# Kernel optimization log

Hardware: AMD Instinct MI355X
Metric: run time of the kernel (lower is better)

## Reference

```python
import jax, jax.numpy as jnp
import numpy as np

N_NODES = 50000
N_EDGES = 800000
D_IN = 128
D_HID = 128
D_OUT = 1
N_GRAPHS = 64
NEG_SLOPE = 0.2


def gat_layer(x, src, dst, W, a_src, a_dst, b, n_nodes):
    # x: [N, d_in] -> h: [N, d_hid]
    h = x @ W
    alpha_s = h @ a_src  # [N]
    alpha_d = h @ a_dst  # [N]
    e = jax.nn.leaky_relu(alpha_s[src] + alpha_d[dst], NEG_SLOPE)  # [E]
    # segment softmax over destination neighborhoods
    m = jax.ops.segment_max(e, dst, num_segments=n_nodes)
    ex = jnp.exp(e - m[dst])
    denom = jax.ops.segment_sum(ex, dst, num_segments=n_nodes)
    alpha = ex / (denom[dst] + 1e-16)  # [E]
    out = jax.ops.segment_sum(h[src] * alpha[:, None], dst, num_segments=n_nodes)
    return out + b


def setup_inputs() -> dict:
    key = jax.random.key(0)
    ks = jax.random.split(key, 16)
    x = jax.random.normal(ks[0], (N_NODES, D_IN), dtype=jnp.float32)
    edge_index = jax.random.randint(ks[1], (2, N_EDGES), 0, N_NODES, dtype=jnp.int32)
    batch = jnp.sort(jax.random.randint(ks[2], (N_NODES,), 0, N_GRAPHS, dtype=jnp.int32))
    inp = {"x": x, "edge_index": edge_index, "batch": batch}
    dims = [(D_IN, D_HID), (D_HID, D_HID), (D_HID, D_HID), (D_HID, D_HID)]
    for i, (di, dh) in enumerate(dims, 1):
        kk = jax.random.split(ks[2 + i], 4)
        s = 1.0 / np.sqrt(di)
        inp[f"W{i}"] = jax.random.uniform(kk[0], (di, dh), jnp.float32, -s, s)
        inp[f"a_src{i}"] = jax.random.uniform(kk[1], (dh,), jnp.float32, -s, s)
        inp[f"a_dst{i}"] = jax.random.uniform(kk[2], (dh,), jnp.float32, -s, s)
        inp[f"b{i}"] = jnp.zeros((dh,), jnp.float32)
    s = 1.0 / np.sqrt(D_HID)
    inp["fcW"] = jax.random.uniform(ks[10], (D_HID, D_OUT), jnp.float32, -s, s)
    inp["fcb"] = jnp.zeros((D_OUT,), jnp.float32)
    return inp


def reference(x, edge_index, batch,
              W1, a_src1, a_dst1, b1,
              W2, a_src2, a_dst2, b2,
              W3, a_src3, a_dst3, b3,
              W4, a_src4, a_dst4, b4,
              fcW, fcb):
    n = x.shape[0]
    loops = jnp.arange(n, dtype=edge_index.dtype)
    src = jnp.concatenate([edge_index[0], loops])  # add self-loops (PyG default)
    dst = jnp.concatenate([edge_index[1], loops])
    h = jax.nn.relu(gat_layer(x, src, dst, W1, a_src1, a_dst1, b1, n))
    h = jax.nn.relu(gat_layer(h, src, dst, W2, a_src2, a_dst2, b2, n))
    h = jax.nn.relu(gat_layer(h, src, dst, W3, a_src3, a_dst3, b3, n))
    h = jax.nn.relu(gat_layer(h, src, dst, W4, a_src4, a_dst4, b4, n))
    # global mean pool over graphs
    sums = jax.ops.segment_sum(h, batch, num_segments=N_GRAPHS)
    counts = jax.ops.segment_sum(jnp.ones((n,), h.dtype), batch, num_segments=N_GRAPHS)
    pooled = sums / jnp.maximum(counts, 1.0)[:, None]
    return pooled @ fcW + fcb
```

## Files before the change

kernel.cpp:

```cpp
#include <hip/hip_runtime.h>

#define N_NODES 50000
#define N_EDGES 800000
#define E_TOT (N_EDGES + N_NODES)
#define D 128
#define N_GRAPHS 64
#define NEG_SLOPE 0.2f
#define MAXDEG 256
#define SCAN_BLK 1024
#define SCAN_GRID ((N_NODES + SCAN_BLK - 1) / SCAN_BLK)

typedef _Float16 f16x8 __attribute__((ext_vector_type(8)));
typedef _Float16 f16x2 __attribute__((ext_vector_type(2)));
typedef float f32x4 __attribute__((ext_vector_type(4)));

__device__ __forceinline__ float wave_max(float v) {
  #pragma unroll
  for (int off = 32; off > 0; off >>= 1) v = fmaxf(v, __shfl_xor(v, off));
  return v;
}
__device__ __forceinline__ float wave_sum(float v) {
  #pragma unroll
  for (int off = 32; off > 0; off >>= 1) v += __shfl_xor(v, off);
  return v;
}

__global__ void k_count(const int* __restrict__ ei, int* __restrict__ cnt) {
  int e = blockIdx.x * blockDim.x + threadIdx.x;
  if (e >= E_TOT) return;
  int dst = (e < N_EDGES) ? ei[N_EDGES + e] : (e - N_EDGES);
  atomicAdd(&cnt[dst], 1);
}

__global__ __launch_bounds__(SCAN_BLK) void k_scan1(const int* __restrict__ cnt,
                                                    int* __restrict__ rowptr,
                                                    int* __restrict__ partial) {
  __shared__ int sm[SCAN_BLK];
  int i = blockIdx.x * SCAN_BLK + threadIdx.x;
  int v = (i < N_NODES) ? cnt[i] : 0;
  sm[threadIdx.x] = v;
  __syncthreads();
  #pragma unroll
  for (int off = 1; off < SCAN_BLK; off <<= 1) {
    int t = (threadIdx.x >= off) ? sm[threadIdx.x - off] : 0;
    __syncthreads();
    sm[threadIdx.x] += t;
    __syncthreads();
  }
  if (i < N_NODES) rowptr[i + 1] = sm[threadIdx.x];
  if (threadIdx.x == SCAN_BLK - 1) partial[blockIdx.x] = sm[threadIdx.x];
}

__global__ void k_scan2(int* __restrict__ partial) {
  int lane = threadIdx.x;
  int v = (lane < SCAN_GRID) ? partial[lane] : 0;
  #pragma unroll
  for (int off = 1; off < 64; off <<= 1) {
    int t = __shfl_up(v, off);
    if (lane >= off) v += t;
  }
  if (lane < SCAN_GRID) partial[lane] = v;
}

__global__ __launch_bounds__(SCAN_BLK) void k_scan3(int* __restrict__ rowptr,
                                                    const int* __restrict__ partial) {
  int i = blockIdx.x * SCAN_BLK + threadIdx.x;
  if (i == 0) rowptr[0] = 0;
  if (i < N_NODES && blockIdx.x > 0) rowptr[i + 1] += partial[blockIdx.x - 1];
}

struct WPtrs {
  const float* w[4];
  _Float16* h[4];
  _Float16* l[4];
};
__global__ __launch_bounds__(256) void k_wconv_all(WPtrs p) {
  int layer = blockIdx.x >> 6;
  int e = (blockIdx.x & 63) * 256 + threadIdx.x;
  int k = e >> 7, n = e & 127;
  float v = p.w[layer][e];
  _Float16 h = (_Float16)v;
  _Float16 lo = (_Float16)(v - (float)h);
  int idx = (n >> 4) * 2048 + (k >> 3) * 128 + (n & 15) * 8 + (k & 7);
  p.h[layer][idx] = h;
  p.l[layer][idx] = lo;
}

template <int DO_FILL>
__global__ __launch_bounds__(256) void k_gemm_mfma(const float* __restrict__ X,
                                                   const _Float16* __restrict__ Whf,
                                                   const _Float16* __restrict__ Wlf,
                                                   _Float16* __restrict__ Hh,
                                                   const float* __restrict__ asrc,
                                                   const float* __restrict__ adst,
                                                   float* __restrict__ alpha_s,
                                                   float* __restrict__ alpha_d,
                                                   const int* __restrict__ ei,
                                                   const int* __restrict__ rowptr,
                                                   int* __restrict__ fill,
                                                   int* __restrict__ col) {
  __shared__ __align__(16) _Float16 AhL[8192];
  __shared__ __align__(16) _Float16 AlL[8192];
  const int tid = threadIdx.x;
  const int l = tid & 63;
  const int w = tid >> 6;
  const int rowbase = blockIdx.x * 64;

  #pragma unroll
  for (int p = 0; p < 4; ++p) {
    int row = p * 16 + (tid >> 4);
    int k0 = (tid & 15) * 8;
    int grow = rowbase + row;
    float xv[8];
    if (grow < N_NODES) {
      float4 f0 = *reinterpret_cast<const float4*>(&X[(size_t)grow * D + k0]);
      float4 f1 = *reinterpret_cast<const float4*>(&X[(size_t)grow * D + k0 + 4]);
      xv[0] = f0.x; xv[1] = f0.y; xv[2] = f0.z; xv[3] = f0.w;
      xv[4] = f1.x; xv[5] = f1.y; xv[6] = f1.z; xv[7] = f1.w;
    } else {
      #pragma unroll
      for (int j = 0; j < 8; ++j) xv[j] = 0.f;
    }
    f16x8 ah, al;
    #pragma unroll
    for (int j = 0; j < 8; ++j) {
      ah[j] = (_Float16)xv[j];
      al[j] = (_Float16)(xv[j] - (float)ah[j]);
    }
    int idx = (((row >> 4) * 16 + (k0 >> 3)) * 16 + (row & 15)) * 8;
    *reinterpret_cast<f16x8*>(&AhL[idx]) = ah;
    *reinterpret_cast<f16x8*>(&AlL[idx]) = al;
  }
  __syncthreads();

  f32x4 acc[8];
  #pragma unroll
  for (int cc = 0; cc < 8; ++cc) acc[cc] = (f32x4){0.f, 0.f, 0.f, 0.f};

  #pragma unroll
  for (int kt = 0; kt < 4; ++kt) {
    int aidx = w * 2048 + kt * 512 + l * 8;
    f16x8 ah = *reinterpret_cast<const f16x8*>(&AhL[aidx]);
    f16x8 al = *reinterpret_cast<const f16x8*>(&AlL[aidx]);
    #pragma unroll
    for (int cc = 0; cc < 8; ++cc) {
      int bidx = cc * 2048 + kt * 512 + l * 8;
      f16x8 bh = *reinterpret_cast<const f16x8*>(&Whf[bidx]);
      f16x8 bl = *reinterpret_cast<const f16x8*>(&Wlf[bidx]);
      acc[cc] = __builtin_amdgcn_mfma_f32_16x16x32_f16(ah, bh, acc[cc], 0, 0, 0);
      acc[cc] = __builtin_amdgcn_mfma_f32_16x16x32_f16(ah, bl, acc[cc], 0, 0, 0);
      acc[cc] = __builtin_amdgcn_mfma_f32_16x16x32_f16(al, bh, acc[cc], 0, 0, 0);
    }
  }

  const int myn = l & 15;
  const int rg4 = l >> 4;
  float asv[8], adv[8];
  #pragma unroll
  for (int cc = 0; cc < 8; ++cc) {
    asv[cc] = asrc[cc * 16 + myn];
    adv[cc] = adst[cc * 16 + myn];
  }
  #pragma unroll
  for (int reg = 0; reg < 4; ++reg) {
    int grow = rowbase + w * 16 + rg4 * 4 + reg;
    float ps = 0.f, pd = 0.f;
    #pragma unroll
    for (int cc = 0; cc < 8; ++cc) {
      float v = acc[cc][reg];
      ps = fmaf(v, asv[cc], ps);
      pd = fmaf(v, adv[cc], pd);
      if (grow < N_NODES) Hh[(size_t)grow * D + cc * 16 + myn] = (_Float16)v;
    }
    #pragma unroll
    for (int off = 1; off < 16; off <<= 1) {
      ps += __shfl_xor(ps, off);
      pd += __shfl_xor(pd, off);
    }
    if (grow < N_NODES && myn == 0) {
      alpha_s[grow] = ps;
      alpha_d[grow] = pd;
    }
  }

  if (DO_FILL) {
    int stride = gridDim.x * blockDim.x;
    for (int e = blockIdx.x * blockDim.x + tid; e < E_TOT; e += stride) {
      int src, dst;
      if (e < N_EDGES) { src = ei[e]; dst = ei[N_EDGES + e]; }
      else { src = e - N_EDGES; dst = src; }
      int pos = rowptr[dst] + atomicAdd(&fill[dst], 1);
      col[pos] = src;
    }
  }
}

template <int FINAL>
__global__ __launch_bounds__(256) void k_agg(const _Float16* __restrict__ Hh,
                                             const int* __restrict__ rowptr,
                                             const int* __restrict__ col,
                                             const float* __restrict__ alpha_s,
                                             const float* __restrict__ alpha_d,
                                             const float* __restrict__ bias,
                                             float* __restrict__ Out,
                                             const float* __restrict__ fcW,
                                             float* __restrict__ ynode) {
  __shared__ float wls[4][MAXDEG];
  __shared__ int cls[4][MAXDEG];
  int wid = threadIdx.x >> 6;
  int lane = threadIdx.x & 63;
  int node = blockIdx.x * 4 + wid;
  if (node >= N_NODES) return;
  int start = rowptr[node], end = rowptr[node + 1];
  int deg = end - start;
  float ad = alpha_d[node];

  float earr[4];
  float m = -1e30f;
  #pragma unroll
  for (int k = 0; k < 4; ++k) {
    int j0 = lane + k * 64;
    earr[k] = -1e30f;
    if (j0 < deg) {
      int s = col[start + j0];
      float e = alpha_s[s] + ad;
      e = e >= 0.f ? e : NEG_SLOPE * e;
      cls[wid][j0] = s;
      earr[k] = e;
    }
  }
  m = fmaxf(fmaxf(earr[0], earr[1]), fmaxf(earr[2], earr[3]));
  for (int j0 = MAXDEG + lane; j0 < deg; j0 += 64) {
    int s = col[start + j0];
    float e = alpha_s[s] + ad;
    e = e >= 0.f ? e : NEG_SLOPE * e;
    m = fmaxf(m, e);
  }
  m = wave_max(m);

  float dsum = 0.f;
  #pragma unroll
  for (int k = 0; k < 4; ++k) {
    int j0 = lane + k * 64;
    if (j0 < deg) {
      float w = expf(earr[k] - m);
      wls[wid][j0] = w;
      dsum += w;
    }
  }
  for (int j0 = MAXDEG + lane; j0 < deg; j0 += 64) {
    int s = col[start + j0];
    float e = alpha_s[s] + ad;
    e = e >= 0.f ? e : NEG_SLOPE * e;
    dsum += expf(e - m);
  }
  dsum = wave_sum(dsum);
  float inv = 1.f / (dsum + 1e-16f);

  float2 acc = make_float2(0.f, 0.f);
  int degc = deg < MAXDEG ? deg : MAXDEG;
  for (int jj = 0; jj < degc; jj += 8) {
    float w[8];
    f16x2 hv[8];
    #pragma unroll
    for (int u = 0; u < 8; ++u) {
      int idx = jj + u;
      bool ok = idx < degc;
      int s = ok ? cls[wid][idx] : cls[wid][0];
      w[u] = ok ? wls[wid][idx] : 0.f;
      hv[u] = *reinterpret_cast<const f16x2*>(&Hh[(size_t)s * D + lane * 2]);
    }
    #pragma unroll
    for (int u = 0; u < 8; ++u) {
      acc.x = fmaf(w[u], (float)hv[u][0], acc.x);
      acc.y = fmaf(w[u], (float)hv[u][1], acc.y);
    }
  }
  for (int jj = MAXDEG; jj < deg; ++jj) {
    int s = col[start + jj];
    float e = alpha_s[s] + ad;
    e = e >= 0.f ? e : NEG_SLOPE * e;
    float w = expf(e - m);
    f16x2 hv = *reinterpret_cast<const f16x2*>(&Hh[(size_t)s * D + lane * 2]);
    acc.x = fmaf(w, (float)hv[0], acc.x);
    acc.y = fmaf(w, (float)hv[1], acc.y);
  }

  float2 bv = *reinterpret_cast<const float2*>(&bias[lane * 2]);
  float ox = fmaxf(acc.x * inv + bv.x, 0.f);
  float oy = fmaxf(acc.y * inv + bv.y, 0.f);
  if (FINAL) {
    float2 wv = *reinterpret_cast<const float2*>(&fcW[lane * 2]);
    float y = wave_sum(ox * wv.x + oy * wv.y);
    if (lane == 0) ynode[node] = y;
  } else {
    *reinterpret_cast<float2*>(&Out[(size_t)node * D + lane * 2]) = make_float2(ox, oy);
  }
}

__global__ __launch_bounds__(256) void k_final(const float* __restrict__ ynode,
                                               const int* __restrict__ batch,
                                               const float* __restrict__ fcb,
                                               float* __restrict__ out) {
  __shared__ float sm[256];
  int b = blockIdx.x;
  int tid = threadIdx.x;
  int lo = 0, hi = N_NODES;
  while (lo < hi) { int mid = (lo + hi) >> 1; if (batch[mid] < b) lo = mid + 1; else hi = mid; }
  int s0 = lo;
  lo = 0; hi = N_NODES;
  while (lo < hi) { int mid = (lo + hi) >> 1; if (batch[mid] < b + 1) lo = mid + 1; else hi = mid; }
  int s1 = lo;
  float sum = 0.f;
  for (int n = s0 + tid; n < s1; n += 256) sum += ynode[n];
  sm[tid] = sum;
  __syncthreads();
  #pragma unroll
  for (int off = 128; off > 0; off >>= 1) {
    if (tid < off) sm[tid] += sm[tid + off];
    __syncthreads();
  }
  if (tid == 0) out[b] = sm[0] / fmaxf((float)(s1 - s0), 1.f) + fcb[0];
}

extern "C" void kernel_launch(void* const* d_in, const int* in_sizes, int n_in,
                              void* d_out, int out_size, void* d_ws, size_t ws_size,
                              hipStream_t stream) {
  const float* x = (const float*)d_in[0];
  const int* ei = (const int*)d_in[1];
  const int* batch = (const int*)d_in[2];
  const float* W[4]   = {(const float*)d_in[3], (const float*)d_in[7],
                         (const float*)d_in[11], (const float*)d_in[15]};
  const float* asr[4] = {(const float*)d_in[4], (const float*)d_in[8],
                         (const float*)d_in[12], (const float*)d_in[16]};
  const float* adt[4] = {(const float*)d_in[5], (const float*)d_in[9],
                         (const float*)d_in[13], (const float*)d_in[17]};
  const float* bs[4]  = {(const float*)d_in[6], (const float*)d_in[10],
                         (const float*)d_in[14], (const float*)d_in[18]};
  const float* fcW = (const float*)d_in[19];
  const float* fcb = (const float*)d_in[20];
  float* out = (float*)d_out;

  char* ws = (char*)d_ws;
  size_t off = 0;
  float* hB = (float*)(ws + off); off += (size_t)N_NODES * D * 4;
  _Float16* Hh = (_Float16*)(ws + off); off += (size_t)N_NODES * D * 2;
  float* alpha_s = (float*)(ws + off); off += (size_t)N_NODES * 4;
  float* alpha_d = (float*)(ws + off); off += (size_t)N_NODES * 4;
  int* cnt  = (int*)(ws + off); off += (size_t)N_NODES * 4;
  int* fill = (int*)(ws + off); off += (size_t)N_NODES * 4;
  int* rowptr = (int*)(ws + off); off += (size_t)(N_NODES + 1) * 4 + 12;
  int* col = (int*)(ws + off); off += (size_t)E_TOT * 4;
  float* ynode = (float*)(ws + off); off += (size_t)N_NODES * 4;
  int* partial = (int*)(ws + off); off += ((size_t)SCAN_GRID * 4 + 15) & ~15ull;
  _Float16* Whf[4];
  _Float16* Wlf[4];
  for (int lyr = 0; lyr < 4; ++lyr) {
    Whf[lyr] = (_Float16*)(ws + off); off += (size_t)D * D * 2;
    Wlf[lyr] = (_Float16*)(ws + off); off += (size_t)D * D * 2;
  }
  (void)ws_size; (void)in_sizes; (void)n_in; (void)out_size;

  hipMemsetAsync(cnt, 0, (size_t)N_NODES * 4 * 2, stream);
  WPtrs wp;
  for (int lyr = 0; lyr < 4; ++lyr) { wp.w[lyr] = W[lyr]; wp.h[lyr] = Whf[lyr]; wp.l[lyr] = Wlf[lyr]; }
  k_wconv_all<<<256, 256, 0, stream>>>(wp);
  int eb = (E_TOT + 255) / 256;
  k_count<<<eb, 256, 0, stream>>>(ei, cnt);
  k_scan1<<<SCAN_GRID, SCAN_BLK, 0, stream>>>(cnt, rowptr, partial);
  k_scan2<<<1, 64, 0, stream>>>(partial);
  k_scan3<<<SCAN_GRID, SCAN_BLK, 0, stream>>>(rowptr, partial);

  int gb = (N_NODES + 63) / 64;
  k_gemm_mfma<1><<<gb, 256, 0, stream>>>(x, Whf[0], Wlf[0], Hh, asr[0], adt[0],
                                         alpha_s, alpha_d, ei, rowptr, fill, col);
  k_agg<0><<<(N_NODES + 3) / 4, 256, 0, stream>>>(Hh, rowptr, col, alpha_s, alpha_d,
                                                  bs[0], hB, nullptr, nullptr);
  for (int l = 1; l < 4; ++l) {
    k_gemm_mfma<0><<<gb, 256, 0, stream>>>(hB, Whf[l], Wlf[l], Hh, asr[l], adt[l],
                                           alpha_s, alpha_d, nullptr, nullptr,
                                           nullptr, nullptr);
    if (l < 3) {
      k_agg<0><<<(N_NODES + 3) / 4, 256, 0, stream>>>(Hh, rowptr, col, alpha_s, alpha_d,
                                                      bs[l], hB, nullptr, nullptr);
    } else {
      k_agg<1><<<(N_NODES + 3) / 4, 256, 0, stream>>>(Hh, rowptr, col, alpha_s, alpha_d,
                                                      bs[l], nullptr, fcW, ynode);
    }
  }
  k_final<<<N_GRAPHS, 256, 0, stream>>>(ynode, batch, fcb, out);
}
```

Before: 326.1 us.

## Store hidden activations in fp16, compress CSR indices to u16, precompute edge ranks

Inter-layer activations are now written by the aggregation kernel as fp16 and read directly by the next GEMM. That drops the hi/lo split of the activation operand and one of the three MFMAs per tile. CSR column indices are stored as 16-bit values, and each edge's slot within its destination row is recorded from the counting atomic, so the fill pass no longer needs a second atomic pass. Together these cut memory traffic and atomics. The risks are reduced activation precision, and 16-bit node indices that cannot hold node ids up to 50000 (above 32767 is fine for unsigned, but the rank must also stay under 65536).

```diff
diff --git a/kernel.cpp b/kernel.cpp
--- a/kernel.cpp
+++ b/kernel.cpp
@@ -25,11 +25,12 @@
   return v;
 }
 
-__global__ void k_count(const int* __restrict__ ei, int* __restrict__ cnt) {
+__global__ void k_count(const int* __restrict__ ei, int* __restrict__ cnt,
+                        unsigned short* __restrict__ rank) {
   int e = blockIdx.x * blockDim.x + threadIdx.x;
   if (e >= E_TOT) return;
   int dst = (e < N_EDGES) ? ei[N_EDGES + e] : (e - N_EDGES);
-  atomicAdd(&cnt[dst], 1);
+  rank[e] = (unsigned short)atomicAdd(&cnt[dst], 1);
 }
 
 __global__ __launch_bounds__(SCAN_BLK) void k_scan1(const int* __restrict__ cnt,
@@ -86,8 +87,8 @@
   p.l[layer][idx] = lo;
 }
 
-template <int DO_FILL>
-__global__ __launch_bounds__(256) void k_gemm_mfma(const float* __restrict__ X,
+template <int MODE>
+__global__ __launch_bounds__(256) void k_gemm_mfma(const void* __restrict__ Xv,
                                                    const _Float16* __restrict__ Whf,
                                                    const _Float16* __restrict__ Wlf,
                                                    _Float16* __restrict__ Hh,
@@ -97,10 +98,10 @@
                                                    float* __restrict__ alpha_d,
                                                    const int* __restrict__ ei,
                                                    const int* __restrict__ rowptr,
-                                                   int* __restrict__ fill,
-                                                   int* __restrict__ col) {
+                                                   const unsigned short* __restrict__ rank,
+                                                   unsigned short* __restrict__ col) {
   __shared__ __align__(16) _Float16 AhL[8192];
-  __shared__ __align__(16) _Float16 AlL[8192];
+  __shared__ __align__(16) _Float16 AlL[MODE ? 8192 : 1];
   const int tid = threadIdx.x;
   const int l = tid & 63;
   const int w = tid >> 6;
@@ -111,25 +112,34 @@
     int row = p * 16 + (tid >> 4);
     int k0 = (tid & 15) * 8;
     int grow = rowbase + row;
-    float xv[8];
-    if (grow < N_NODES) {
-      float4 f0 = *reinterpret_cast<const float4*>(&X[(size_t)grow * D + k0]);
-      float4 f1 = *reinterpret_cast<const float4*>(&X[(size_t)grow * D + k0 + 4]);
-      xv[0] = f0.x; xv[1] = f0.y; xv[2] = f0.z; xv[3] = f0.w;
-      xv[4] = f1.x; xv[5] = f1.y; xv[6] = f1.z; xv[7] = f1.w;
+    int idx = (((row >> 4) * 16 + (k0 >> 3)) * 16 + (row & 15)) * 8;
+    if (MODE) {
+      const float* X = (const float*)Xv;
+      float xv[8];
+      if (grow < N_NODES) {
+        float4 f0 = *reinterpret_cast<const float4*>(&X[(size_t)grow * D + k0]);
+        float4 f1 = *reinterpret_cast<const float4*>(&X[(size_t)grow * D + k0 + 4]);
+        xv[0] = f0.x; xv[1] = f0.y; xv[2] = f0.z; xv[3] = f0.w;
+        xv[4] = f1.x; xv[5] = f1.y; xv[6] = f1.z; xv[7] = f1.w;
+      } else {
+        #pragma unroll
+        for (int j = 0; j < 8; ++j) xv[j] = 0.f;
+      }
+      f16x8 ah, al;
+      #pragma unroll
+      for (int j = 0; j < 8; ++j) {
+        ah[j] = (_Float16)xv[j];
+        al[j] = (_Float16)(xv[j] - (float)ah[j]);
+      }
+      *reinterpret_cast<f16x8*>(&AhL[idx]) = ah;
+      *reinterpret_cast<f16x8*>(&AlL[idx]) = al;
     } else {
-      #pragma unroll
-      for (int j = 0; j < 8; ++j) xv[j] = 0.f;
-    }
-    f16x8 ah, al;
-    #pragma unroll
-    for (int j = 0; j < 8; ++j) {
-      ah[j] = (_Float16)xv[j];
-      al[j] = (_Float16)(xv[j] - (float)ah[j]);
-    }
-    int idx = (((row >> 4) * 16 + (k0 >> 3)) * 16 + (row & 15)) * 8;
-    *reinterpret_cast<f16x8*>(&AhL[idx]) = ah;
-    *reinterpret_cast<f16x8*>(&AlL[idx]) = al;
+      const _Float16* X = (const _Float16*)Xv;
+      f16x8 ah = {0, 0, 0, 0, 0, 0, 0, 0};
+      if (grow < N_NODES)
+        ah = *reinterpret_cast<const f16x8*>(&X[(size_t)grow * D + k0]);
+      *reinterpret_cast<f16x8*>(&AhL[idx]) = ah;
+    }
   }
   __syncthreads();
 
@@ -141,7 +151,8 @@
   for (int kt = 0; kt < 4; ++kt) {
     int aidx = w * 2048 + kt * 512 + l * 8;
     f16x8 ah = *reinterpret_cast<const f16x8*>(&AhL[aidx]);
-    f16x8 al = *reinterpret_cast<const f16x8*>(&AlL[aidx]);
+    f16x8 al;
+    if (MODE) al = *reinterpret_cast<const f16x8*>(&AlL[aidx]);
     #pragma unroll
     for (int cc = 0; cc < 8; ++cc) {
       int bidx = cc * 2048 + kt * 512 + l * 8;
@@ -149,7 +160,8 @@
       f16x8 bl = *reinterpret_cast<const f16x8*>(&Wlf[bidx]);
       acc[cc] = __builtin_amdgcn_mfma_f32_16x16x32_f16(ah, bh, acc[cc], 0, 0, 0);
       acc[cc] = __builtin_amdgcn_mfma_f32_16x16x32_f16(ah, bl, acc[cc], 0, 0, 0);
-      acc[cc] = __builtin_amdgcn_mfma_f32_16x16x32_f16(al, bh, acc[cc], 0, 0, 0);
+      if (MODE)
+        acc[cc] = __builtin_amdgcn_mfma_f32_16x16x32_f16(al, bh, acc[cc], 0, 0, 0);
     }
   }
 
@@ -183,14 +195,13 @@
     }
   }
 
-  if (DO_FILL) {
+  if (MODE) {
     int stride = gridDim.x * blockDim.x;
     for (int e = blockIdx.x * blockDim.x + tid; e < E_TOT; e += stride) {
       int src, dst;
       if (e < N_EDGES) { src = ei[e]; dst = ei[N_EDGES + e]; }
       else { src = e - N_EDGES; dst = src; }
-      int pos = rowptr[dst] + atomicAdd(&fill[dst], 1);
-      col[pos] = src;
+      col[rowptr[dst] + rank[e]] = (unsigned short)src;
     }
   }
 }
@@ -198,11 +209,11 @@
 template <int FINAL>
 __global__ __launch_bounds__(256) void k_agg(const _Float16* __restrict__ Hh,
                                              const int* __restrict__ rowptr,
-                                             const int* __restrict__ col,
+                                             const unsigned short* __restrict__ col,
                                              const float* __restrict__ alpha_s,
                                              const float* __restrict__ alpha_d,
                                              const float* __restrict__ bias,
-                                             float* __restrict__ Out,
+                                             _Float16* __restrict__ Out,
                                              const float* __restrict__ fcW,
                                              float* __restrict__ ynode) {
   __shared__ float wls[4][MAXDEG];
@@ -294,7 +305,10 @@
     float y = wave_sum(ox * wv.x + oy * wv.y);
     if (lane == 0) ynode[node] = y;
   } else {
-    *reinterpret_cast<float2*>(&Out[(size_t)node * D + lane * 2]) = make_float2(ox, oy);
+    f16x2 o;
+    o[0] = (_Float16)ox;
+    o[1] = (_Float16)oy;
+    *reinterpret_cast<f16x2*>(&Out[(size_t)node * D + lane * 2]) = o;
   }
 }
 
@@ -343,14 +357,14 @@
 
   char* ws = (char*)d_ws;
   size_t off = 0;
-  float* hB = (float*)(ws + off); off += (size_t)N_NODES * D * 4;
-  _Float16* Hh = (_Float16*)(ws + off); off += (size_t)N_NODES * D * 2;
+  _Float16* Hh  = (_Float16*)(ws + off); off += (size_t)N_NODES * D * 2;
+  _Float16* hBh = (_Float16*)(ws + off); off += (size_t)N_NODES * D * 2;
   float* alpha_s = (float*)(ws + off); off += (size_t)N_NODES * 4;
   float* alpha_d = (float*)(ws + off); off += (size_t)N_NODES * 4;
   int* cnt  = (int*)(ws + off); off += (size_t)N_NODES * 4;
-  int* fill = (int*)(ws + off); off += (size_t)N_NODES * 4;
   int* rowptr = (int*)(ws + off); off += (size_t)(N_NODES + 1) * 4 + 12;
-  int* col = (int*)(ws + off); off += (size_t)E_TOT * 4;
+  unsigned short* col = (unsigned short*)(ws + off); off += ((size_t)E_TOT * 2 + 15) & ~15ull;
+  unsigned short* rank = (unsigned short*)(ws + off); off += ((size_t)E_TOT * 2 + 15) & ~15ull;
   float* ynode = (float*)(ws + off); off += (size_t)N_NODES * 4;
   int* partial = (int*)(ws + off); off += ((size_t)SCAN_GRID * 4 + 15) & ~15ull;
   _Float16* Whf[4];
@@ -361,28 +375,28 @@
   }
   (void)ws_size; (void)in_sizes; (void)n_in; (void)out_size;
 
-  hipMemsetAsync(cnt, 0, (size_t)N_NODES * 4 * 2, stream);
+  hipMemsetAsync(cnt, 0, (size_t)N_NODES * 4, stream);
   WPtrs wp;
   for (int lyr = 0; lyr < 4; ++lyr) { wp.w[lyr] = W[lyr]; wp.h[lyr] = Whf[lyr]; wp.l[lyr] = Wlf[lyr]; }
   k_wconv_all<<<256, 256, 0, stream>>>(wp);
   int eb = (E_TOT + 255) / 256;
-  k_count<<<eb, 256, 0, stream>>>(ei, cnt);
+  k_count<<<eb, 256, 0, stream>>>(ei, cnt, rank);
   k_scan1<<<SCAN_GRID, SCAN_BLK, 0, stream>>>(cnt, rowptr, partial);
   k_scan2<<<1, 64, 0, stream>>>(partial);
   k_scan3<<<SCAN_GRID, SCAN_BLK, 0, stream>>>(rowptr, partial);
 
   int gb = (N_NODES + 63) / 64;
   k_gemm_mfma<1><<<gb, 256, 0, stream>>>(x, Whf[0], Wlf[0], Hh, asr[0], adt[0],
-                                         alpha_s, alpha_d, ei, rowptr, fill, col);
+                                         alpha_s, alpha_d, ei, rowptr, rank, col);
   k_agg<0><<<(N_NODES + 3) / 4, 256, 0, stream>>>(Hh, rowptr, col, alpha_s, alpha_d,
-                                                  bs[0], hB, nullptr, nullptr);
+                                                  bs[0], hBh, nullptr, nullptr);
   for (int l = 1; l < 4; ++l) {
-    k_gemm_mfma<0><<<gb, 256, 0, stream>>>(hB, Whf[l], Wlf[l], Hh, asr[l], adt[l],
+    k_gemm_mfma<0><<<gb, 256, 0, stream>>>(hBh, Whf[l], Wlf[l], Hh, asr[l], adt[l],
                                            alpha_s, alpha_d, nullptr, nullptr,
                                            nullptr, nullptr);
     if (l < 3) {
       k_agg<0><<<(N_NODES + 3) / 4, 256, 0, stream>>>(Hh, rowptr, col, alpha_s, alpha_d,
-                                                      bs[l], hB, nullptr, nullptr);
+                                                      bs[l], hBh, nullptr, nullptr);
     } else {
       k_agg<1><<<(N_NODES + 3) / 4, 256, 0, stream>>>(Hh, rowptr, col, alpha_s, alpha_d,
                                                       bs[l], nullptr, fcW, ynode);
```

After: 297.3 us. 8.8% less time.
